# Kernel tuning notes

Hardware: AMD Instinct MI355X
Metric: run time of the kernel (lower is better)

The kernel has to match this reference:

```python
import jax, jax.numpy as jnp
import numpy as np

B, N, E, H, DIN, DB, P, L, NB = 2, 10000, 100000, 128, 8, 16, 3, 2, 3


def setup_inputs() -> dict:
    key = jax.random.key(0)
    ks = jax.random.split(key, 16)

    def rn(i, shape, s=0.05):
        return jax.random.normal(ks[i], shape, dtype=jnp.float32) * s

    return {
        "x": jax.random.normal(ks[0], (B, DIN), dtype=jnp.float32),
        "base_features": rn(1, (N, DB), 1.0),
        "base_positions": rn(2, (N, P), 1.0),
        "Win": rn(3, (DB + DIN, H)),
        "b_in": jnp.zeros((H,), jnp.float32),
        "msg_W1": rn(4, (L, NB, 2 * H + 1, H)),
        "msg_b1": jnp.zeros((L, NB, H), jnp.float32),
        "msg_W2": rn(5, (L, NB, H, H)),
        "msg_b2": jnp.zeros((L, NB, H), jnp.float32),
        "pos_W1": rn(6, (L, NB, H, H)),
        "pos_b1": jnp.zeros((L, NB, H), jnp.float32),
        "pos_W2": rn(7, (L, NB, H, 1)),
        "pos_b2": jnp.zeros((L, NB, 1), jnp.float32),
        "upd_W1": rn(8, (L, 2 * H, H)),
        "upd_b1": jnp.zeros((L, H), jnp.float32),
        "upd_W2": rn(9, (L, H, H)),
        "upd_b2": jnp.zeros((L, H), jnp.float32),
        "out_W1": rn(10, (H, H)),
        "out_b1": jnp.zeros((H,), jnp.float32),
        "out_W2": rn(11, (H, 1)),
        "out_b2": jnp.zeros((1,), jnp.float32),
        "entity_indices": jax.random.randint(ks[12], (B,), 0, N),
        "edge_src": jax.random.randint(ks[13], (NB, E), 0, N),
        "edge_dst": jax.random.randint(ks[14], (NB, E), 0, N),
    }


def reference(x, base_features, base_positions, Win, b_in,
              msg_W1, msg_b1, msg_W2, msg_b2,
              pos_W1, pos_b1, pos_W2, pos_b2,
              upd_W1, upd_b1, upd_W2, upd_b2,
              out_W1, out_b1, out_W2, out_b2,
              entity_indices, edge_src, edge_dst):
    silu = jax.nn.silu
    b = x.shape[0]
    n = base_features.shape[0]
    # scatter each batch element's dynamic features onto its entity cell
    dynamic = jnp.zeros((b, n, x.shape[1]), x.dtype).at[jnp.arange(b), entity_indices].set(x)
    base = jnp.broadcast_to(base_features[None], (b, n, base_features.shape[1]))
    h = jnp.concatenate([base, dynamic], axis=-1) @ Win + b_in          # [B,N,H]
    p = jnp.broadcast_to(base_positions[None], (b, n, base_positions.shape[1]))  # [B,N,3]
    n_layers, n_nbhd = msg_W1.shape[0], edge_src.shape[0]
    for l in range(n_layers):
        m_sum = jnp.zeros_like(h)
        p_new = p
        for k in range(n_nbhd):
            src, dst = edge_src[k], edge_dst[k]
            # degree of aggregation target (matches torch bincount over indices[1])
            deg = jnp.clip(jnp.zeros((n,), h.dtype).at[dst].add(1.0), 1.0)[None, :, None]
            rel = p[:, dst] - p[:, src]                                  # [B,E,3]
            d2 = jnp.sum(rel * rel, axis=-1, keepdims=True)              # [B,E,1]
            m = silu(jnp.concatenate([h[:, dst], h[:, src], d2], axis=-1) @ msg_W1[l, k] + msg_b1[l, k])
            m = silu(m @ msg_W2[l, k] + msg_b2[l, k])                    # [B,E,H]
            m_sum = m_sum + jnp.zeros_like(h).at[:, dst].add(m) / deg
            coef = silu(m @ pos_W1[l, k] + pos_b1[l, k]) @ pos_W2[l, k] + pos_b2[l, k]  # [B,E,1]
            p_new = p_new + jnp.zeros_like(p).at[:, dst].add(rel * coef) / deg
        h = h + (silu(jnp.concatenate([h, m_sum], axis=-1) @ upd_W1[l] + upd_b1[l]) @ upd_W2[l] + upd_b2[l])
        p = p_new
    e = h[jnp.arange(b), entity_indices]                                 # [B,H] gather readout
    return silu(e @ out_W1 + out_b1) @ out_W2 + out_b2                   # [B,1]
```

## Files before the change

kernel.cpp:

```cpp
#include <hip/hip_runtime.h>
#include <hip/hip_bf16.h>
#include <math.h>

#define Bc   2
#define Nc   10000
#define Ec   100000
#define Hc   128
#define DINc 8
#define DBc  16
#define NBc  3
#define Lc   2

typedef float v4 __attribute__((ext_vector_type(4)));
typedef float f32x16 __attribute__((ext_vector_type(16)));
typedef _Float16 h8 __attribute__((ext_vector_type(8)));
typedef _Float16 h4 __attribute__((ext_vector_type(4)));

__device__ __forceinline__ float silu_f(float x) {
  return x * __builtin_amdgcn_rcpf(1.f + __expf(-x));
}

__device__ __forceinline__ h4 pack4(float a, float b, float c, float d) {
  typedef decltype(__builtin_amdgcn_cvt_pkrtz(0.f, 0.f)) pk2;
  union { h4 v; pk2 p[2]; } u;
  u.p[0] = __builtin_amdgcn_cvt_pkrtz(a, b);
  u.p[1] = __builtin_amdgcn_cvt_pkrtz(c, d);
  return u.v;
}


__global__ void zero4_kernel(float* __restrict__ p, int n4) {
  int i = blockIdx.x * blockDim.x + threadIdx.x;
  if (i < n4) ((v4*)p)[i] = (v4)(0.f);
}

__global__ void copy_kernel(float* __restrict__ dst, const float* __restrict__ src, int n) {
  int i = blockIdx.x * blockDim.x + threadIdx.x;
  if (i < n) dst[i] = src[i];
}


__global__ void hist_kernel(int* __restrict__ hist, const int* __restrict__ edst) {
  int i = blockIdx.x * blockDim.x + threadIdx.x;
  if (i < NBc * Ec) {
    int k = i / Ec;
    atomicAdd(&hist[k * Nc + edst[i]], 1);
  }
}

__global__ void scan_kernel(const int* __restrict__ hist, int* __restrict__ offs,
                            float* __restrict__ deginv) {
  const int k = blockIdx.x, tid = threadIdx.x;
  const int NPT = 40;
  __shared__ int part[256];
  int local[NPT];
  int sum = 0;
  for (int j = 0; j < NPT; ++j) {
    int n = tid * NPT + j;
    if (n < Nc) { local[j] = sum; sum += hist[k * Nc + n]; }
  }
  part[tid] = sum;
  __syncthreads();
  for (int off = 1; off < 256; off <<= 1) {
    int v = (tid >= off) ? part[tid - off] : 0;
    __syncthreads();
    part[tid] += v;
    __syncthreads();
  }
  int excl = part[tid] - sum;
  for (int j = 0; j < NPT; ++j) {
    int n = tid * NPT + j;
    if (n < Nc) {
      offs[k * Nc + n] = excl + local[j];
      deginv[k * Nc + n] = 1.f / fmaxf((float)hist[k * Nc + n], 1.f);
    }
  }
}

__global__ void sort_scatter_kernel(int* __restrict__ sorted, int* __restrict__ cursor,
                                    const int* __restrict__ offs, const int* __restrict__ edst) {
  int i = blockIdx.x * blockDim.x + threadIdx.x;
  if (i < NBc * Ec) {
    int k = i / Ec, e = i - k * Ec;
    int d = edst[i];
    int pos = offs[k * Nc + d] + atomicAdd(&cursor[k * Nc + d], 1);
    sorted[k * Ec + pos] = e;
  }
}


__global__ void init_h_kernel(_Float16* __restrict__ h16, const float* __restrict__ bfeat,
                              const float* __restrict__ x, const float* __restrict__ Win,
                              const float* __restrict__ b_in, const int* __restrict__ ent) {
  int g = blockIdx.x * blockDim.x + threadIdx.x;
  if (g >= Bc * Nc * Hc) return;
  int j = g & (Hc - 1);
  int bn = g >> 7;
  int n = bn % Nc;
  int b = bn / Nc;
  float acc = b_in[j];
#pragma unroll
  for (int i = 0; i < DBc; ++i) acc = fmaf(bfeat[n * DBc + i], Win[i * Hc + j], acc);
  if (n == ent[b]) {
#pragma unroll
    for (int i = 0; i < DINc; ++i) acc = fmaf(x[b * DINc + i], Win[(DBc + i) * Hc + j], acc);
  }
  h16[g] = (_Float16)acc;
}

__global__ void init_p_kernel(float* __restrict__ p, const float* __restrict__ bp) {
  int i = blockIdx.x * blockDim.x + threadIdx.x;
  if (i < Bc * Nc * 3) p[i] = bp[i % (Nc * 3)];
}

__global__ void conv_ext_kernel(_Float16* __restrict__ dst, const float* __restrict__ src,
                                const float* __restrict__ bias,
                                int nchunk, int total, int realRows, int biasRow) {
  int g = blockIdx.x * blockDim.x + threadIdx.x;
  if (g >= total) return;
  int j = g & 7;
  int lane = (g >> 3) & 63;
  int q = g >> 9;
  int t = q % nchunk;
  int q2 = q / nchunk;
  int wave = q2 & 3;
  int mat = q2 >> 2;
  int kk = t * 16 + (lane >> 5) * 8 + j;
  int col = (wave << 5) + (lane & 31);
  float v = 0.f;
  if (kk < realRows)      v = src[((size_t)mat * realRows + kk) * Hc + col];
  else if (kk == biasRow) v = bias[mat * Hc + col];
  dst[g] = (_Float16)v;
}


__global__ __launch_bounds__(256, 4)
void edge_mfma_kernel(const _Float16* __restrict__ h16, const float* __restrict__ p,
                      float* __restrict__ m_sum, float* __restrict__ p_new,
                      const float* __restrict__ deginv,
                      const int* __restrict__ esrc, const int* __restrict__ edst,
                      const int* __restrict__ sorted,
                      const _Float16* __restrict__ W1e, const _Float16* __restrict__ W2e,
                      const _Float16* __restrict__ P1e,
                      const float* __restrict__ pW2, const float* __restrict__ pb2,
                      int l) {
  const int k = blockIdx.y, lk = l * NBc + k;
  const int tid = threadIdx.x;
  const int wave = tid >> 6, lane = tid & 63;
  const int lrow = lane & 31, lhalf = lane >> 5;

  __shared__ __align__(16) _Float16 RegA[16384];
  __shared__ __align__(16) _Float16 Dchk[1024];
  __shared__ int shd[64], shs[64], sOff[64];
  __shared__ float sdinv[64], srel[64][3], scoef[64];
  __shared__ float cpw2[Hc];
  __shared__ unsigned long long sflush;

  if (tid < Hc) cpw2[tid] = pW2[lk * Hc + tid];
  if (tid < 64) {
    int pos = blockIdx.x * 64 + tid;
    int b = (pos >= Ec) ? 1 : 0;
    int e = sorted[k * Ec + (pos - b * Ec)];
    int si = esrc[k * Ec + e], di = edst[k * Ec + e];
    int nd = b * Nc + di, ns = b * Nc + si;
    const float* pd = &p[(size_t)nd * 3];
    const float* ps = &p[(size_t)ns * 3];
    float rx = pd[0] - ps[0], ry = pd[1] - ps[1], rz = pd[2] - ps[2];
    srel[tid][0] = rx; srel[tid][1] = ry; srel[tid][2] = rz;
    float d2 = rx * rx + ry * ry + rz * rz;
    sdinv[tid] = deginv[k * Nc + di];
    shd[tid] = nd * Hc; shs[tid] = ns * Hc;
    sOff[tid] = nd * Hc;
    scoef[tid] = 0.f;
    h8 dv = (h8)(_Float16)0.f;
    h8 zv = (h8)(_Float16)0.f;
    dv[0] = (_Float16)d2; dv[1] = (_Float16)1.f;
    int g = tid >> 5, il = tid & 31;
    *(h8*)&Dchk[g * 512 + il * 8] = dv;
    *(h8*)&Dchk[g * 512 + 256 + il * 8] = zv;
    int prevn = __shfl_up(nd, 1);
    bool isStart = (tid == 0) || (nd != prevn);
    unsigned long long m = __ballot(isStart);
    if (tid == 0) sflush = (m >> 1) | (1ull << 63);
  }
  __syncthreads();

  {
    const int i = tid & 63, cg = tid >> 6;
    const int g = i >> 5, il = i & 31;
#pragma unroll
    for (int q = 0; q < 4; ++q) {
      int d0 = cg * 32 + q * 8;
      int t = d0 >> 4;
      int kh = q & 1;
      h8 vd = *(const h8*)&h16[shd[i] + d0];
      h8 vs = *(const h8*)&h16[shs[i] + d0];
      *(h8*)&RegA[(t * 2 + g) * 512 + kh * 256 + il * 8] = vd;
      *(h8*)&RegA[((8 + t) * 2 + g) * 512 + kh * 256 + il * 8] = vs;
    }
  }
  __syncthreads();

  const _Float16* wb1 = &W1e[(size_t)(lk * 4 + wave) * (17 * 512)];
  f32x16 aA, aB;
#pragma unroll
  for (int r = 0; r < 16; ++r) { aA[r] = 0.f; aB[r] = 0.f; }
#pragma unroll
  for (int t = 0; t < 16; ++t) {
    h8 aw = *(const h8*)&wb1[t * 512 + lane * 8];
    h8 bA = *(const h8*)&RegA[(t * 2 + 0) * 512 + lane * 8];
    h8 bB = *(const h8*)&RegA[(t * 2 + 1) * 512 + lane * 8];
    aA = __builtin_amdgcn_mfma_f32_32x32x16_f16(aw, bA, aA, 0, 0, 0);
    aB = __builtin_amdgcn_mfma_f32_32x32x16_f16(aw, bB, aB, 0, 0, 0);
  }
  {
    h8 aw = *(const h8*)&wb1[16 * 512 + lane * 8];
    h8 dA = *(const h8*)&Dchk[lane * 8];
    h8 dB = *(const h8*)&Dchk[512 + lane * 8];
    aA = __builtin_amdgcn_mfma_f32_32x32x16_f16(aw, dA, aA, 0, 0, 0);
    aB = __builtin_amdgcn_mfma_f32_32x32x16_f16(aw, dB, aB, 0, 0, 0);
  }
  h4 m1A[4], m1B[4];
#pragma unroll
  for (int c = 0; c < 4; ++c) {
    m1A[c] = pack4(silu_f(aA[c * 4 + 0]), silu_f(aA[c * 4 + 1]),
                   silu_f(aA[c * 4 + 2]), silu_f(aA[c * 4 + 3]));
    m1B[c] = pack4(silu_f(aB[c * 4 + 0]), silu_f(aB[c * 4 + 1]),
                   silu_f(aB[c * 4 + 2]), silu_f(aB[c * 4 + 3]));
  }
  __syncthreads();
#pragma unroll
  for (int c = 0; c < 4; ++c) {
    int t = 2 * wave + (c >> 1);
    int base = (c & 1) * 256 + lrow * 8 + lhalf * 4;
    *(h4*)&RegA[(t * 2 + 0) * 512 + base] = m1A[c];
    *(h4*)&RegA[(t * 2 + 1) * 512 + base] = m1B[c];
  }
  __syncthreads();

  const _Float16* wb2 = &W2e[(size_t)(lk * 4 + wave) * (9 * 512)];
#pragma unroll
  for (int r = 0; r < 16; ++r) { aA[r] = 0.f; aB[r] = 0.f; }
#pragma unroll
  for (int t = 0; t < 8; ++t) {
    h8 aw = *(const h8*)&wb2[t * 512 + lane * 8];
    h8 bA = *(const h8*)&RegA[(t * 2 + 0) * 512 + lane * 8];
    h8 bB = *(const h8*)&RegA[(t * 2 + 1) * 512 + lane * 8];
    aA = __builtin_amdgcn_mfma_f32_32x32x16_f16(aw, bA, aA, 0, 0, 0);
    aB = __builtin_amdgcn_mfma_f32_32x32x16_f16(aw, bB, aB, 0, 0, 0);
  }
  {
    h8 aw = *(const h8*)&wb2[8 * 512 + lane * 8];
    h8 dA = *(const h8*)&Dchk[lane * 8];
    h8 dB = *(const h8*)&Dchk[512 + lane * 8];
    aA = __builtin_amdgcn_mfma_f32_32x32x16_f16(aw, dA, aA, 0, 0, 0);
    aB = __builtin_amdgcn_mfma_f32_32x32x16_f16(aw, dB, aB, 0, 0, 0);
  }
#pragma unroll
  for (int c = 0; c < 4; ++c) {
    h4 p2A = pack4(silu_f(aA[c * 4 + 0]), silu_f(aA[c * 4 + 1]),
                   silu_f(aA[c * 4 + 2]), silu_f(aA[c * 4 + 3]));
    h4 p2B = pack4(silu_f(aB[c * 4 + 0]), silu_f(aB[c * 4 + 1]),
                   silu_f(aB[c * 4 + 2]), silu_f(aB[c * 4 + 3]));
    int t2 = 8 + 2 * wave + (c >> 1);
    int base = (c & 1) * 256 + lrow * 8 + lhalf * 4;
    *(h4*)&RegA[(t2 * 2 + 0) * 512 + base] = p2A;
    *(h4*)&RegA[(t2 * 2 + 1) * 512 + base] = p2B;
  }
  __syncthreads();

  const _Float16* wb3 = &P1e[(size_t)(lk * 4 + wave) * (9 * 512)];
#pragma unroll
  for (int r = 0; r < 16; ++r) { aA[r] = 0.f; aB[r] = 0.f; }
#pragma unroll
  for (int t = 0; t < 8; ++t) {
    h8 aw = *(const h8*)&wb3[t * 512 + lane * 8];
    h8 bA = *(const h8*)&RegA[((8 + t) * 2 + 0) * 512 + lane * 8];
    h8 bB = *(const h8*)&RegA[((8 + t) * 2 + 1) * 512 + lane * 8];
    aA = __builtin_amdgcn_mfma_f32_32x32x16_f16(aw, bA, aA, 0, 0, 0);
    aB = __builtin_amdgcn_mfma_f32_32x32x16_f16(aw, bB, aB, 0, 0, 0);
  }
  {
    h8 aw = *(const h8*)&wb3[8 * 512 + lane * 8];
    h8 dA = *(const h8*)&Dchk[lane * 8];
    h8 dB = *(const h8*)&Dchk[512 + lane * 8];
    aA = __builtin_amdgcn_mfma_f32_32x32x16_f16(aw, dA, aA, 0, 0, 0);
    aB = __builtin_amdgcn_mfma_f32_32x32x16_f16(aw, dB, aB, 0, 0, 0);
  }
  {
    float csA = 0.f, csB = 0.f;
#pragma unroll
    for (int r = 0; r < 16; ++r) {
      int hg = (wave << 5) + (r & 3) + ((r >> 2) << 3) + (lhalf << 2);
      csA += silu_f(aA[r]) * cpw2[hg];
      csB += silu_f(aB[r]) * cpw2[hg];
    }
    csA += __shfl_down(csA, 32);
    csB += __shfl_down(csB, 32);
    if (lane < 32) {
      atomicAdd(&scoef[lrow], csA);
      atomicAdd(&scoef[32 + lrow], csB);
    }
  }

  {
    const int col = tid & 127;
    const int half = tid >> 7;
    const int base = ((8 + (col >> 4)) * 2 + half) * 512 + ((col >> 3) & 1) * 256 + (col & 7);
    const unsigned long long fm = sflush;
    float accv = 0.f;
#pragma unroll
    for (int rr = 0; rr < 32; ++rr) {
      int r = half * 32 + rr;
      accv += (float)RegA[base + rr * 8];
      if ((fm >> r) & 1ull) {
        atomicAdd(&m_sum[sOff[r] + col], accv * sdinv[r]);
        accv = 0.f;
      }
    }
    if (half == 0 && !((fm >> 31) & 1ull))
      atomicAdd(&m_sum[sOff[31] + col], accv * sdinv[31]);
  }
  __syncthreads();
  if (tid < 64) {
    float cf = (scoef[tid] + pb2[lk]) * sdinv[tid];
    float* pp = &p_new[(size_t)(sOff[tid] / Hc) * 3];
    atomicAdd(&pp[0], srel[tid][0] * cf);
    atomicAdd(&pp[1], srel[tid][1] * cf);
    atomicAdd(&pp[2], srel[tid][2] * cf);
  }
}


__global__ __launch_bounds__(256, 8)
void update_mfma_kernel(_Float16* __restrict__ h16, const float* __restrict__ m_sum,
                        const _Float16* __restrict__ U1e, const _Float16* __restrict__ U2e,
                        int l) {
  const int tid = threadIdx.x;
  const int wave = tid >> 6, lane = tid & 63;
  const int lrow = lane & 31, lhalf = lane >> 5;
  const int row0 = blockIdx.x << 5;

  __shared__ __align__(16) _Float16 RegA[16 * 512];
  __shared__ __align__(16) _Float16 Dchk[512];

  if (tid < 64) {
    h8 dv = (h8)(_Float16)0.f;
    if (tid < 32) dv[1] = (_Float16)1.f;
    *(h8*)&Dchk[tid * 8] = dv;
  }
  {
    const int i = tid & 31, c = tid >> 5;
    size_t hb = (size_t)(row0 + i) * Hc;
    h8 v0 = *(const h8*)&h16[hb + c * 8];
    h8 v1 = *(const h8*)&h16[hb + 64 + c * 8];
    v4 m0 = *(const v4*)&m_sum[hb + c * 8];
    v4 m1 = *(const v4*)&m_sum[hb + c * 8 + 4];
    v4 m2 = *(const v4*)&m_sum[hb + 64 + c * 8];
    v4 m3 = *(const v4*)&m_sum[hb + 64 + c * 8 + 4];
    union { h8 v; h4 q[2]; } w0, w1;
    w0.q[0] = pack4(m0[0], m0[1], m0[2], m0[3]);
    w0.q[1] = pack4(m1[0], m1[1], m1[2], m1[3]);
    w1.q[0] = pack4(m2[0], m2[1], m2[2], m2[3]);
    w1.q[1] = pack4(m3[0], m3[1], m3[2], m3[3]);
    int slot = (i + ((c & 1) << 5)) << 3;
    int tb = (c >> 1) << 9;
    *(h8*)&RegA[tb + slot] = v0;
    *(h8*)&RegA[tb + 4 * 512 + slot] = v1;
    *(h8*)&RegA[tb + 8 * 512 + slot] = w0.v;
    *(h8*)&RegA[tb + 12 * 512 + slot] = w1.v;
  }
  __syncthreads();

  const _Float16* wb1 = &U1e[(size_t)(l * 4 + wave) * (17 * 512)];
  f32x16 acc;
#pragma unroll
  for (int r = 0; r < 16; ++r) acc[r] = 0.f;
#pragma unroll
  for (int t = 0; t < 16; ++t) {
    h8 bact = *(const h8*)&RegA[t * 512 + lane * 8];
    h8 aw   = *(const h8*)&wb1[t * 512 + lane * 8];
    acc = __builtin_amdgcn_mfma_f32_32x32x16_f16(aw, bact, acc, 0, 0, 0);
  }
  {
    h8 bact = *(const h8*)&Dchk[lane * 8];
    h8 aw   = *(const h8*)&wb1[16 * 512 + lane * 8];
    acc = __builtin_amdgcn_mfma_f32_32x32x16_f16(aw, bact, acc, 0, 0, 0);
  }
  h4 u1pk[4];
#pragma unroll
  for (int c = 0; c < 4; ++c)
    u1pk[c] = pack4(silu_f(acc[c * 4 + 0]), silu_f(acc[c * 4 + 1]),
                    silu_f(acc[c * 4 + 2]), silu_f(acc[c * 4 + 3]));
  __syncthreads();
#pragma unroll
  for (int c = 0; c < 4; ++c) {
    int t = (wave << 1) + (c >> 1);
    int slot = lrow + ((c & 1) << 5);
    *(h4*)&RegA[t * 512 + slot * 8 + lhalf * 4] = u1pk[c];
  }
  __syncthreads();

  const _Float16* wb2 = &U2e[(size_t)(l * 4 + wave) * (9 * 512)];
  f32x16 acc2;
#pragma unroll
  for (int r = 0; r < 16; ++r) acc2[r] = 0.f;
#pragma unroll
  for (int t = 0; t < 8; ++t) {
    h8 bact = *(const h8*)&RegA[t * 512 + lane * 8];
    h8 aw   = *(const h8*)&wb2[t * 512 + lane * 8];
    acc2 = __builtin_amdgcn_mfma_f32_32x32x16_f16(aw, bact, acc2, 0, 0, 0);
  }
  {
    h8 bact = *(const h8*)&Dchk[lane * 8];
    h8 aw   = *(const h8*)&wb2[8 * 512 + lane * 8];
    acc2 = __builtin_amdgcn_mfma_f32_32x32x16_f16(aw, bact, acc2, 0, 0, 0);
  }
  {
    _Float16* hp = &h16[(size_t)(row0 + lrow) * Hc];
#pragma unroll
    for (int c = 0; c < 4; ++c) {
      int hb = (wave << 5) + (c << 3) + (lhalf << 2);
      h4 old = *(const h4*)&hp[hb];
      *(h4*)&hp[hb] = pack4((float)old[0] + acc2[c * 4 + 0], (float)old[1] + acc2[c * 4 + 1],
                            (float)old[2] + acc2[c * 4 + 2], (float)old[3] + acc2[c * 4 + 3]);
    }
  }
}


__global__ void readout_kernel(const _Float16* __restrict__ h16, const int* __restrict__ ent,
                               const float* __restrict__ oW1, const float* __restrict__ ob1,
                               const float* __restrict__ oW2, const float* __restrict__ ob2,
                               float* __restrict__ out) {
  __shared__ float tb[Bc][Hc];
  int tid = threadIdx.x;
  int b = tid >> 7, j = tid & 127;
  const _Float16* e = &h16[((size_t)(b * Nc + ent[b])) * Hc];
  float a = ob1[j];
#pragma unroll 4
  for (int i = 0; i < Hc; ++i) a = fmaf((float)e[i], oW1[i * Hc + j], a);
  tb[b][j] = silu_f(a);
  __syncthreads();
  if (tid < Bc) {
    float s = ob2[0];
    for (int i = 0; i < Hc; ++i) s = fmaf(tb[tid][i], oW2[i], s);
    out[tid] = s;
  }
}


extern "C" void kernel_launch(void* const* d_in, const int* in_sizes, int n_in,
                              void* d_out, int out_size, void* d_ws, size_t ws_size,
                              hipStream_t stream) {
  const float* x    = (const float*)d_in[0];
  const float* bfe  = (const float*)d_in[1];
  const float* bp   = (const float*)d_in[2];
  const float* Win  = (const float*)d_in[3];
  const float* b_in = (const float*)d_in[4];
  const float* mW1  = (const float*)d_in[5];
  const float* mb1  = (const float*)d_in[6];
  const float* mW2  = (const float*)d_in[7];
  const float* mb2  = (const float*)d_in[8];
  const float* pW1  = (const float*)d_in[9];
  const float* pb1  = (const float*)d_in[10];
  const float* pW2  = (const float*)d_in[11];
  const float* pb2  = (const float*)d_in[12];
  const float* uW1  = (const float*)d_in[13];
  const float* ub1  = (const float*)d_in[14];
  const float* uW2  = (const float*)d_in[15];
  const float* ub2  = (const float*)d_in[16];
  const float* oW1  = (const float*)d_in[17];
  const float* ob1  = (const float*)d_in[18];
  const float* oW2  = (const float*)d_in[19];
  const float* ob2  = (const float*)d_in[20];
  const int* ent    = (const int*)d_in[21];
  const int* esrc   = (const int*)d_in[22];
  const int* edst   = (const int*)d_in[23];

  float* wsf = (float*)d_ws;
  float* msum   = wsf;  wsf += (size_t)Bc * Nc * Hc;
  float* pa     = wsf;  wsf += (size_t)Bc * Nc * 3;
  float* pb_    = wsf;  wsf += (size_t)Bc * Nc * 3;
  float* deginv = wsf;  wsf += (size_t)NBc * Nc;
  _Float16* h16 = (_Float16*)wsf;
  _Float16* W1e = h16 + (size_t)Bc * Nc * Hc;
  _Float16* W2e = W1e + 208896;
  _Float16* P1e = W2e + 110592;
  _Float16* U1e = P1e + 110592;
  _Float16* U2e = U1e + 69632;
  int* hist   = (int*)(U2e + 36864);
  int* cursor = hist + NBc * Nc;
  int* offs   = cursor + NBc * Nc;
  int* sorted = offs + NBc * Nc;

  zero4_kernel<<<dim3((2 * NBc * Nc / 4 + 255) / 256), dim3(256), 0, stream>>>((float*)hist, 2 * NBc * Nc / 4);
  hist_kernel<<<dim3((NBc * Ec + 255) / 256), dim3(256), 0, stream>>>(hist, edst);
  scan_kernel<<<dim3(NBc), dim3(256), 0, stream>>>(hist, offs, deginv);
  sort_scatter_kernel<<<dim3((NBc * Ec + 255) / 256), dim3(256), 0, stream>>>(sorted, cursor, offs, edst);

  conv_ext_kernel<<<dim3(816), dim3(256), 0, stream>>>(W1e, mW1, mb1, 17, 208896, 257, 257);
  conv_ext_kernel<<<dim3(432), dim3(256), 0, stream>>>(W2e, mW2, mb2, 9, 110592, 128, 129);
  conv_ext_kernel<<<dim3(432), dim3(256), 0, stream>>>(P1e, pW1, pb1, 9, 110592, 128, 129);
  conv_ext_kernel<<<dim3(272), dim3(256), 0, stream>>>(U1e, uW1, ub1, 17, 69632, 256, 257);
  conv_ext_kernel<<<dim3(144), dim3(256), 0, stream>>>(U2e, uW2, ub2, 9, 36864, 128, 129);

  init_h_kernel<<<dim3((Bc * Nc * Hc + 255) / 256), dim3(256), 0, stream>>>(h16, bfe, x, Win, b_in, ent);
  init_p_kernel<<<dim3((Bc * Nc * 3 + 255) / 256), dim3(256), 0, stream>>>(pa, bp);

  float* pcur = pa;
  float* pnew = pb_;
  const int nmh = Bc * Nc * Hc;
  for (int l = 0; l < Lc; ++l) {
    zero4_kernel<<<dim3((nmh / 4 + 255) / 256), dim3(256), 0, stream>>>(msum, nmh / 4);
    copy_kernel<<<dim3((Bc * Nc * 3 + 255) / 256), dim3(256), 0, stream>>>(pnew, pcur, Bc * Nc * 3);
    edge_mfma_kernel<<<dim3(Bc * Ec / 64, NBc), dim3(256), 0, stream>>>(
        h16, pcur, msum, pnew, deginv, esrc, edst, sorted,
        W1e, W2e, P1e, pW2, pb2, l);
    update_mfma_kernel<<<dim3(Bc * Nc / 32), dim3(256), 0, stream>>>(h16, msum, U1e, U2e, l);
    float* t = pcur; pcur = pnew; pnew = t;
  }
  readout_kernel<<<dim3(1), dim3(256), 0, stream>>>(h16, ent, oW1, ob1, oW2, ob2, (float*)d_out);
}
```

Baseline: 669.6 us.

## Preload MFMA weight fragments into registers and double-buffer activations to drop barriers

Both the edge and update kernels now load all per-wave weight fragments into registers at kernel start, so the global weight loads are issued early and overlap the gather phase. Separate LDS buffers (Mbuf, plus a swizzled RMbuf for the message reduction) remove the extra __syncthreads that guarded in-place reuse of RegA, and the swizzle targets LDS bank conflicts in the column reduction. To fit the much higher register and LDS use, launch bounds drop from 4 to 2 blocks per SM for the edge kernel and from 8 to 3 for the update kernel, which lowers occupancy and risks worse latency hiding.

```diff
diff --git a/kernel.cpp b/kernel.cpp
--- a/kernel.cpp
+++ b/kernel.cpp
@@ -134,7 +134,7 @@
 }
 
 
-__global__ __launch_bounds__(256, 4)
+__global__ __launch_bounds__(256, 2)
 void edge_mfma_kernel(const _Float16* __restrict__ h16, const float* __restrict__ p,
                       float* __restrict__ m_sum, float* __restrict__ p_new,
                       const float* __restrict__ deginv,
@@ -150,11 +150,24 @@
   const int lrow = lane & 31, lhalf = lane >> 5;
 
   __shared__ __align__(16) _Float16 RegA[16384];
+  __shared__ __align__(16) _Float16 Mbuf[8192];
+  __shared__ __align__(16) _Float16 RMbuf[8192];
   __shared__ __align__(16) _Float16 Dchk[1024];
-  __shared__ int shd[64], shs[64], sOff[64];
+  __shared__ int shd[64], shs[64], snd[64];
   __shared__ float sdinv[64], srel[64][3], scoef[64];
   __shared__ float cpw2[Hc];
   __shared__ unsigned long long sflush;
+
+  const _Float16* wb1 = &W1e[(size_t)(lk * 4 + wave) * (17 * 512)];
+  const _Float16* wb2 = &W2e[(size_t)(lk * 4 + wave) * (9 * 512)];
+  const _Float16* wb3 = &P1e[(size_t)(lk * 4 + wave) * (9 * 512)];
+  h8 w1r[17], w2r[9], w3r[9];
+#pragma unroll
+  for (int t = 0; t < 17; ++t) w1r[t] = *(const h8*)&wb1[t * 512 + lane * 8];
+#pragma unroll
+  for (int t = 0; t < 9; ++t)  w2r[t] = *(const h8*)&wb2[t * 512 + lane * 8];
+#pragma unroll
+  for (int t = 0; t < 9; ++t)  w3r[t] = *(const h8*)&wb3[t * 512 + lane * 8];
 
   if (tid < Hc) cpw2[tid] = pW2[lk * Hc + tid];
   if (tid < 64) {
@@ -169,8 +182,7 @@
     srel[tid][0] = rx; srel[tid][1] = ry; srel[tid][2] = rz;
     float d2 = rx * rx + ry * ry + rz * rz;
     sdinv[tid] = deginv[k * Nc + di];
-    shd[tid] = nd * Hc; shs[tid] = ns * Hc;
-    sOff[tid] = nd * Hc;
+    shd[tid] = nd * Hc; shs[tid] = ns * Hc; snd[tid] = nd;
     scoef[tid] = 0.f;
     h8 dv = (h8)(_Float16)0.f;
     h8 zv = (h8)(_Float16)0.f;
@@ -185,6 +197,9 @@
   }
   __syncthreads();
 
+  h8 dA = *(const h8*)&Dchk[lane * 8];
+  h8 dB = *(const h8*)&Dchk[512 + lane * 8];
+
   {
     const int i = tid & 63, cg = tid >> 6;
     const int g = i >> 5, il = i & 31;
@@ -201,92 +216,73 @@
   }
   __syncthreads();
 
-  const _Float16* wb1 = &W1e[(size_t)(lk * 4 + wave) * (17 * 512)];
   f32x16 aA, aB;
 #pragma unroll
   for (int r = 0; r < 16; ++r) { aA[r] = 0.f; aB[r] = 0.f; }
 #pragma unroll
   for (int t = 0; t < 16; ++t) {
-    h8 aw = *(const h8*)&wb1[t * 512 + lane * 8];
     h8 bA = *(const h8*)&RegA[(t * 2 + 0) * 512 + lane * 8];
     h8 bB = *(const h8*)&RegA[(t * 2 + 1) * 512 + lane * 8];
-    aA = __builtin_amdgcn_mfma_f32_32x32x16_f16(aw, bA, aA, 0, 0, 0);
-    aB = __builtin_amdgcn_mfma_f32_32x32x16_f16(aw, bB, aB, 0, 0, 0);
-  }
-  {
-    h8 aw = *(const h8*)&wb1[16 * 512 + lane * 8];
-    h8 dA = *(const h8*)&Dchk[lane * 8];
-    h8 dB = *(const h8*)&Dchk[512 + lane * 8];
-    aA = __builtin_amdgcn_mfma_f32_32x32x16_f16(aw, dA, aA, 0, 0, 0);
-    aB = __builtin_amdgcn_mfma_f32_32x32x16_f16(aw, dB, aB, 0, 0, 0);
-  }
-  h4 m1A[4], m1B[4];
+    aA = __builtin_amdgcn_mfma_f32_32x32x16_f16(w1r[t], bA, aA, 0, 0, 0);
+    aB = __builtin_amdgcn_mfma_f32_32x32x16_f16(w1r[t], bB, aB, 0, 0, 0);
+  }
+  aA = __builtin_amdgcn_mfma_f32_32x32x16_f16(w1r[16], dA, aA, 0, 0, 0);
+  aB = __builtin_amdgcn_mfma_f32_32x32x16_f16(w1r[16], dB, aB, 0, 0, 0);
 #pragma unroll
   for (int c = 0; c < 4; ++c) {
-    m1A[c] = pack4(silu_f(aA[c * 4 + 0]), silu_f(aA[c * 4 + 1]),
+    h4 m1A = pack4(silu_f(aA[c * 4 + 0]), silu_f(aA[c * 4 + 1]),
                    silu_f(aA[c * 4 + 2]), silu_f(aA[c * 4 + 3]));
-    m1B[c] = pack4(silu_f(aB[c * 4 + 0]), silu_f(aB[c * 4 + 1]),
+    h4 m1B = pack4(silu_f(aB[c * 4 + 0]), silu_f(aB[c * 4 + 1]),
                    silu_f(aB[c * 4 + 2]), silu_f(aB[c * 4 + 3]));
-  }
-  __syncthreads();
-#pragma unroll
-  for (int c = 0; c < 4; ++c) {
     int t = 2 * wave + (c >> 1);
     int base = (c & 1) * 256 + lrow * 8 + lhalf * 4;
-    *(h4*)&RegA[(t * 2 + 0) * 512 + base] = m1A[c];
-    *(h4*)&RegA[(t * 2 + 1) * 512 + base] = m1B[c];
-  }
-  __syncthreads();
-
-  const _Float16* wb2 = &W2e[(size_t)(lk * 4 + wave) * (9 * 512)];
+    *(h4*)&Mbuf[(t * 2 + 0) * 512 + base] = m1A;
+    *(h4*)&Mbuf[(t * 2 + 1) * 512 + base] = m1B;
+  }
+  __syncthreads();
+
 #pragma unroll
   for (int r = 0; r < 16; ++r) { aA[r] = 0.f; aB[r] = 0.f; }
 #pragma unroll
   for (int t = 0; t < 8; ++t) {
-    h8 aw = *(const h8*)&wb2[t * 512 + lane * 8];
-    h8 bA = *(const h8*)&RegA[(t * 2 + 0) * 512 + lane * 8];
-    h8 bB = *(const h8*)&RegA[(t * 2 + 1) * 512 + lane * 8];
-    aA = __builtin_amdgcn_mfma_f32_32x32x16_f16(aw, bA, aA, 0, 0, 0);
-    aB = __builtin_amdgcn_mfma_f32_32x32x16_f16(aw, bB, aB, 0, 0, 0);
-  }
+    h8 bA = *(const h8*)&Mbuf[(t * 2 + 0) * 512 + lane * 8];
+    h8 bB = *(const h8*)&Mbuf[(t * 2 + 1) * 512 + lane * 8];
+    aA = __builtin_amdgcn_mfma_f32_32x32x16_f16(w2r[t], bA, aA, 0, 0, 0);
+    aB = __builtin_amdgcn_mfma_f32_32x32x16_f16(w2r[t], bB, aB, 0, 0, 0);
+  }
+  aA = __builtin_amdgcn_mfma_f32_32x32x16_f16(w2r[8], dA, aA, 0, 0, 0);
+  aB = __builtin_amdgcn_mfma_f32_32x32x16_f16(w2r[8], dB, aB, 0, 0, 0);
   {
-    h8 aw = *(const h8*)&wb2[8 * 512 + lane * 8];
-    h8 dA = *(const h8*)&Dchk[lane * 8];
-    h8 dB = *(const h8*)&Dchk[512 + lane * 8];
-    aA = __builtin_amdgcn_mfma_f32_32x32x16_f16(aw, dA, aA, 0, 0, 0);
-    aB = __builtin_amdgcn_mfma_f32_32x32x16_f16(aw, dB, aB, 0, 0, 0);
-  }
-#pragma unroll
-  for (int c = 0; c < 4; ++c) {
-    h4 p2A = pack4(silu_f(aA[c * 4 + 0]), silu_f(aA[c * 4 + 1]),
-                   silu_f(aA[c * 4 + 2]), silu_f(aA[c * 4 + 3]));
-    h4 p2B = pack4(silu_f(aB[c * 4 + 0]), silu_f(aB[c * 4 + 1]),
-                   silu_f(aB[c * 4 + 2]), silu_f(aB[c * 4 + 3]));
-    int t2 = 8 + 2 * wave + (c >> 1);
-    int base = (c & 1) * 256 + lrow * 8 + lhalf * 4;
-    *(h4*)&RegA[(t2 * 2 + 0) * 512 + base] = p2A;
-    *(h4*)&RegA[(t2 * 2 + 1) * 512 + base] = p2B;
-  }
-  __syncthreads();
-
-  const _Float16* wb3 = &P1e[(size_t)(lk * 4 + wave) * (9 * 512)];
+    char* rm = (char*)RMbuf;
+#pragma unroll
+    for (int c = 0; c < 4; ++c) {
+      h4 p2A = pack4(silu_f(aA[c * 4 + 0]), silu_f(aA[c * 4 + 1]),
+                     silu_f(aA[c * 4 + 2]), silu_f(aA[c * 4 + 3]));
+      h4 p2B = pack4(silu_f(aB[c * 4 + 0]), silu_f(aB[c * 4 + 1]),
+                     silu_f(aB[c * 4 + 2]), silu_f(aB[c * 4 + 3]));
+      int t2 = 8 + 2 * wave + (c >> 1);
+      int base = (c & 1) * 256 + lrow * 8 + lhalf * 4;
+      *(h4*)&RegA[(t2 * 2 + 0) * 512 + base] = p2A;
+      *(h4*)&RegA[(t2 * 2 + 1) * 512 + base] = p2B;
+      int hb = (wave << 5) + (c << 3) + (lhalf << 2);
+      int sw = (lrow & 15) << 4;
+      *(h4*)(rm + (lrow << 8) + (((hb << 1)) ^ sw)) = p2A;
+      *(h4*)(rm + ((32 + lrow) << 8) + (((hb << 1)) ^ sw)) = p2B;
+    }
+  }
+  __syncthreads();
+
 #pragma unroll
   for (int r = 0; r < 16; ++r) { aA[r] = 0.f; aB[r] = 0.f; }
 #pragma unroll
   for (int t = 0; t < 8; ++t) {
-    h8 aw = *(const h8*)&wb3[t * 512 + lane * 8];
     h8 bA = *(const h8*)&RegA[((8 + t) * 2 + 0) * 512 + lane * 8];
     h8 bB = *(const h8*)&RegA[((8 + t) * 2 + 1) * 512 + lane * 8];
-    aA = __builtin_amdgcn_mfma_f32_32x32x16_f16(aw, bA, aA, 0, 0, 0);
-    aB = __builtin_amdgcn_mfma_f32_32x32x16_f16(aw, bB, aB, 0, 0, 0);
-  }
-  {
-    h8 aw = *(const h8*)&wb3[8 * 512 + lane * 8];
-    h8 dA = *(const h8*)&Dchk[lane * 8];
-    h8 dB = *(const h8*)&Dchk[512 + lane * 8];
-    aA = __builtin_amdgcn_mfma_f32_32x32x16_f16(aw, dA, aA, 0, 0, 0);
-    aB = __builtin_amdgcn_mfma_f32_32x32x16_f16(aw, dB, aB, 0, 0, 0);
-  }
+    aA = __builtin_amdgcn_mfma_f32_32x32x16_f16(w3r[t], bA, aA, 0, 0, 0);
+    aB = __builtin_amdgcn_mfma_f32_32x32x16_f16(w3r[t], bB, aB, 0, 0, 0);
+  }
+  aA = __builtin_amdgcn_mfma_f32_32x32x16_f16(w3r[8], dA, aA, 0, 0, 0);
+  aB = __builtin_amdgcn_mfma_f32_32x32x16_f16(w3r[8], dB, aB, 0, 0, 0);
   {
     float csA = 0.f, csB = 0.f;
 #pragma unroll
@@ -306,25 +302,26 @@
   {
     const int col = tid & 127;
     const int half = tid >> 7;
-    const int base = ((8 + (col >> 4)) * 2 + half) * 512 + ((col >> 3) & 1) * 256 + (col & 7);
     const unsigned long long fm = sflush;
+    const char* rm = (const char*)RMbuf;
     float accv = 0.f;
 #pragma unroll
     for (int rr = 0; rr < 32; ++rr) {
       int r = half * 32 + rr;
-      accv += (float)RegA[base + rr * 8];
+      float v = (float)*(const _Float16*)(rm + (r << 8) + (((col << 1)) ^ ((r & 15) << 4)));
+      accv += v;
       if ((fm >> r) & 1ull) {
-        atomicAdd(&m_sum[sOff[r] + col], accv * sdinv[r]);
+        atomicAdd(&m_sum[snd[r] * Hc + col], accv * sdinv[r]);
         accv = 0.f;
       }
     }
     if (half == 0 && !((fm >> 31) & 1ull))
-      atomicAdd(&m_sum[sOff[31] + col], accv * sdinv[31]);
+      atomicAdd(&m_sum[snd[31] * Hc + col], accv * sdinv[31]);
   }
   __syncthreads();
   if (tid < 64) {
     float cf = (scoef[tid] + pb2[lk]) * sdinv[tid];
-    float* pp = &p_new[(size_t)(sOff[tid] / Hc) * 3];
+    float* pp = &p_new[(size_t)snd[tid] * 3];
     atomicAdd(&pp[0], srel[tid][0] * cf);
     atomicAdd(&pp[1], srel[tid][1] * cf);
     atomicAdd(&pp[2], srel[tid][2] * cf);
@@ -332,7 +329,7 @@
 }
 
 
-__global__ __launch_bounds__(256, 8)
+__global__ __launch_bounds__(256, 3)
 void update_mfma_kernel(_Float16* __restrict__ h16, const float* __restrict__ m_sum,
                         const _Float16* __restrict__ U1e, const _Float16* __restrict__ U2e,
                         int l) {
@@ -342,7 +339,16 @@
   const int row0 = blockIdx.x << 5;
 
   __shared__ __align__(16) _Float16 RegA[16 * 512];
+  __shared__ __align__(16) _Float16 Mbuf[8 * 512];
   __shared__ __align__(16) _Float16 Dchk[512];
+
+  const _Float16* ub1 = &U1e[(size_t)(l * 4 + wave) * (17 * 512)];
+  const _Float16* ub2 = &U2e[(size_t)(l * 4 + wave) * (9 * 512)];
+  h8 u1r[17], u2r[9];
+#pragma unroll
+  for (int t = 0; t < 17; ++t) u1r[t] = *(const h8*)&ub1[t * 512 + lane * 8];
+#pragma unroll
+  for (int t = 0; t < 9; ++t)  u2r[t] = *(const h8*)&ub2[t * 512 + lane * 8];
 
   if (tid < 64) {
     h8 dv = (h8)(_Float16)0.f;
@@ -372,50 +378,36 @@
   }
   __syncthreads();
 
-  const _Float16* wb1 = &U1e[(size_t)(l * 4 + wave) * (17 * 512)];
+  h8 dR = *(const h8*)&Dchk[lane * 8];
+
   f32x16 acc;
 #pragma unroll
   for (int r = 0; r < 16; ++r) acc[r] = 0.f;
 #pragma unroll
   for (int t = 0; t < 16; ++t) {
     h8 bact = *(const h8*)&RegA[t * 512 + lane * 8];
-    h8 aw   = *(const h8*)&wb1[t * 512 + lane * 8];
-    acc = __builtin_amdgcn_mfma_f32_32x32x16_f16(aw, bact, acc, 0, 0, 0);
-  }
-  {
-    h8 bact = *(const h8*)&Dchk[lane * 8];
-    h8 aw   = *(const h8*)&wb1[16 * 512 + lane * 8];
-    acc = __builtin_amdgcn_mfma_f32_32x32x16_f16(aw, bact, acc, 0, 0, 0);
-  }
-  h4 u1pk[4];
-#pragma unroll
-  for (int c = 0; c < 4; ++c)
-    u1pk[c] = pack4(silu_f(acc[c * 4 + 0]), silu_f(acc[c * 4 + 1]),
+    acc = __builtin_amdgcn_mfma_f32_32x32x16_f16(u1r[t], bact, acc, 0, 0, 0);
+  }
+  acc = __builtin_amdgcn_mfma_f32_32x32x16_f16(u1r[16], dR, acc, 0, 0, 0);
+#pragma unroll
+  for (int c = 0; c < 4; ++c) {
+    h4 u1pk = pack4(silu_f(acc[c * 4 + 0]), silu_f(acc[c * 4 + 1]),
                     silu_f(acc[c * 4 + 2]), silu_f(acc[c * 4 + 3]));
-  __syncthreads();
-#pragma unroll
-  for (int c = 0; c < 4; ++c) {
     int t = (wave << 1) + (c >> 1);
-    int slot = lrow + ((c & 1) << 5);
-    *(h4*)&RegA[t * 512 + slot * 8 + lhalf * 4] = u1pk[c];
-  }
-  __syncthreads();
-
-  const _Float16* wb2 = &U2e[(size_t)(l * 4 + wave) * (9 * 512)];
+    int base = (c & 1) * 256 + lrow * 8 + lhalf * 4;
+    *(h4*)&Mbuf[t * 512 + base] = u1pk;
+  }
+  __syncthreads();
+
   f32x16 acc2;
 #pragma unroll
   for (int r = 0; r < 16; ++r) acc2[r] = 0.f;
 #pragma unroll
   for (int t = 0; t < 8; ++t) {
-    h8 bact = *(const h8*)&RegA[t * 512 + lane * 8];
-    h8 aw   = *(const h8*)&wb2[t * 512 + lane * 8];
-    acc2 = __builtin_amdgcn_mfma_f32_32x32x16_f16(aw, bact, acc2, 0, 0, 0);
-  }
-  {
-    h8 bact = *(const h8*)&Dchk[lane * 8];
-    h8 aw   = *(const h8*)&wb2[8 * 512 + lane * 8];
-    acc2 = __builtin_amdgcn_mfma_f32_32x32x16_f16(aw, bact, acc2, 0, 0, 0);
-  }
+    h8 bact = *(const h8*)&Mbuf[t * 512 + lane * 8];
+    acc2 = __builtin_amdgcn_mfma_f32_32x32x16_f16(u2r[t], bact, acc2, 0, 0, 0);
+  }
+  acc2 = __builtin_amdgcn_mfma_f32_32x32x16_f16(u2r[8], dR, acc2, 0, 0, 0);
   {
     _Float16* hp = &h16[(size_t)(row0 + lrow) * Hc];
 #pragma unroll
```

Measured after the change: 777.9 us. +16.2%, slower.
